# Performance work log

Measured on AMD Instinct MI355X. Metric: run time of the kernel, lower is better.

The kernel has to match this reference:

```python
import jax, jax.numpy as jnp
import numpy as np

N_NODES = 8192
K = 32

def setup_inputs() -> dict:
    key = jax.random.key(0)
    kA, kI = jax.random.split(key)
    A = jax.random.normal(kA, (N_NODES, N_NODES), dtype=jnp.float32)
    idx = jnp.arange(N_NODES, dtype=jnp.int64)  # unused by forward, kept for signature fidelity
    return {"A": A, "idx": idx}

def reference(A, idx):
    # adj = relu(A)
    adj = jax.nn.relu(A)
    # row-wise top-k indices, scatter 1.0 into a zero mask, multiply
    _, indices = jax.lax.top_k(adj, K)            # [N, K]
    rows = jnp.arange(adj.shape[0])[:, None]      # [N, 1]
    mask = jnp.zeros_like(adj).at[rows, indices].set(1.0)
    return adj * mask
```

## Files before the change

kernel.cpp:

```cpp
#include <hip/hip_runtime.h>


constexpr int N     = 8192;
constexpr int K     = 32;
constexpr int NBINS = 2048;
constexpr int SPEC_BASE = 1024;
constexpr int CAP   = 512;
constexpr int SLOTS = CAP / 64;
constexpr int BB    = 128;
constexpr int BLOCK = 256;
constexpr float TSPEC = 2.0f;

typedef float f4 __attribute__((ext_vector_type(4)));

template<int PER>
__device__ __forceinline__ bool find_cutoff(const unsigned* hist, int lane,
                                            int base, int& B, int& G) {
    unsigned s = 0;
    #pragma unroll
    for (int i = 0; i < PER; ++i)
        s += hist[base + lane * PER + ((i + lane) & (PER - 1))];
    unsigned acc = s;
    #pragma unroll
    for (int off = 1; off < 64; off <<= 1) {
        unsigned t = __shfl_down(acc, off, 64);
        if (lane + off < 64) acc += t;
    }
    unsigned long long m = __ballot(acc >= (unsigned)K);
    if (m == 0ull) return false;
    int g = 63 - __clzll((long long)m);
    unsigned above = (g < 63) ? (unsigned)__shfl((int)acc, g + 1, 64) : 0u;
    unsigned h  = (lane < PER) ? hist[base + g * PER + lane] : 0u;
    unsigned a2 = h;
    #pragma unroll
    for (int off = 1; off < 64; off <<= 1) {
        unsigned t = __shfl_down(a2, off, 64);
        if (lane + off < 64) a2 += t;
    }
    unsigned long long m2 = __ballot(above + a2 >= (unsigned)K);
    int bl = 63 - __clzll((long long)m2);
    B = base + g * PER + bl;
    G = (int)(above + (unsigned)__shfl((int)a2, bl, 64)
                    - (unsigned)__shfl((int)h,  bl, 64));
    return true;
}

__global__ __launch_bounds__(BLOCK)
void topk_relu_kernel(const float* __restrict__ A, float* __restrict__ Out) {
    const int row  = blockIdx.x;
    const int tid  = threadIdx.x;
    const int lane = tid & 63;
    const int wave = tid >> 6;

    __shared__ unsigned hist[NBINS];
    __shared__ float    cv[CAP];
    __shared__ int      cc[CAP];
    __shared__ float    bbv[BB];
    __shared__ int      bbc[BB];
    __shared__ unsigned ccnt;

    #pragma unroll
    for (int i = 0; i < (NBINS - SPEC_BASE) / BLOCK; ++i)
        hist[SPEC_BASE + tid + i * BLOCK] = 0u;
    if (tid == 0) ccnt = 0u;
    __syncthreads();

    const f4* __restrict__ Arow = reinterpret_cast<const f4*>(A + (size_t)row * N);
    #pragma unroll
    for (int i = 0; i < 8; ++i) {
        f4 v = Arow[i * BLOCK + tid];
        #pragma unroll
        for (int c = 0; c < 4; ++c) {
            float f = v[c];
            if (f > TSPEC) {
                atomicAdd(&hist[__float_as_uint(f) >> 20], 1u);
                unsigned ix = atomicAdd(&ccnt, 1u);
                if (ix < CAP) { cv[ix] = f; cc[ix] = (i * BLOCK + tid) * 4 + c; }
            }
        }
    }
    __syncthreads();

    int B, G;
    bool ok = find_cutoff<16>(hist, lane, SPEC_BASE, B, G);
    const unsigned Call = ccnt;
    f4* __restrict__ Orow4 = reinterpret_cast<f4*>(Out + (size_t)row * N);

    if (ok && Call <= (unsigned)CAP) {
        const f4 z = {0.0f, 0.0f, 0.0f, 0.0f};
        #pragma unroll
        for (int i = 0; i < 8; ++i)
            __builtin_nontemporal_store(z, Orow4 + i * BLOCK + tid);

        const int R = K - G;
        const int C = (int)Call;
        int total = 0;
        #pragma unroll
        for (int s = 0; s < SLOTS; ++s) {
            const int j = lane + s * 64;
            bool flag = false; float fv = 0.0f; int fc = 0;
            if (j < C) {
                fv = cv[j];
                if ((int)(__float_as_uint(fv) >> 20) == B) { flag = true; fc = cc[j]; }
            }
            unsigned long long m = __ballot(flag);
            if (flag) {
                int pos = total + __popcll(m & ((1ull << lane) - 1ull));
                if (pos < BB) { bbv[pos] = fv; bbc[pos] = fc; }
            }
            total += (int)__popcll(m);
        }
        const int T = min(total, BB);
        float mv0 = -1.0f, mv1 = -1.0f; int mc0 = 0x7fffffff, mc1 = 0x7fffffff;
        if (lane      < T) { mv0 = bbv[lane];      mc0 = bbc[lane]; }
        if (lane + 64 < T) { mv1 = bbv[lane + 64]; mc1 = bbc[lane + 64]; }
        int r0 = 0, r1 = 0;
        for (int j = 0; j < T; ++j) {
            const float vj = bbv[j];
            const int   cj = bbc[j];
            if (vj > mv0 || (vj == mv0 && cj < mc0)) r0++;
            if (vj > mv1 || (vj == mv1 && cj < mc1)) r1++;
        }
        float bv = 0.0f; int bc = -1; bool found = false;
        if (lane      < T && r0 == R - 1) { bv = mv0; bc = mc0; found = true; }
        if (lane + 64 < T && r1 == R - 1) { bv = mv1; bc = mc1; found = true; }
        float vR = __int_as_float(0x7f800000);
        int   cR = -1;
        unsigned long long bm = __ballot(found);
        if (bm != 0ull) {
            int src = (int)__ffsll((long long)bm) - 1;
            vR = __shfl(bv, src, 64);
            cR = __shfl(bc, src, 64);
        }

        __syncthreads();

        if (wave == 0) {
            float* __restrict__ Orow = Out + (size_t)row * N;
            #pragma unroll
            for (int s = 0; s < SLOTS; ++s) {
                const int j = lane + s * 64;
                if (j < C) {
                    float f = cv[j]; int c = cc[j];
                    if (f > vR || (f == vR && c <= cR)) Orow[c] = f;
                }
            }
        }
        return;
    }

    __syncthreads();
    #pragma unroll
    for (int i = 0; i < NBINS / BLOCK; ++i) hist[tid + i * BLOCK] = 0u;
    if (tid == 0) ccnt = 0u;
    __syncthreads();
    #pragma unroll
    for (int i = 0; i < 8; ++i) {
        f4 v = Arow[i * BLOCK + tid];
        #pragma unroll
        for (int c = 0; c < 4; ++c) {
            float f = v[c];
            if (f > 0.0f) atomicAdd(&hist[__float_as_uint(f) >> 20], 1u);
        }
    }
    __syncthreads();
    if (!find_cutoff<32>(hist, lane, 0, B, G)) { B = -1; G = 0; }
    if (B >= 0) {
        #pragma unroll
        for (int i = 0; i < 8; ++i) {
            f4 v = Arow[i * BLOCK + tid];
            #pragma unroll
            for (int c = 0; c < 4; ++c) {
                float f = v[c];
                if (f > 0.0f && (int)(__float_as_uint(f) >> 20) == B) {
                    unsigned ix = atomicAdd(&ccnt, 1u);
                    if (ix < CAP) { cv[ix] = f; cc[ix] = (i * BLOCK + tid) * 4 + c; }
                }
            }
        }
    }
    __syncthreads();

    float vR = 0.0f;
    int   cR = -1;
    if (B >= 0) {
        const int R = K - G;
        const int C = (int)min(ccnt, (unsigned)CAP);
        float mv[SLOTS]; int mc[SLOTS]; int rk[SLOTS];
        #pragma unroll
        for (int s = 0; s < SLOTS; ++s) {
            const int j = lane + s * 64;
            if (j < C) { mv[s] = cv[j]; mc[s] = cc[j]; }
            else       { mv[s] = -1.0f; mc[s] = 0x7fffffff; }
            rk[s] = 0;
        }
        for (int j = 0; j < C; ++j) {
            const float vj = cv[j];
            const int   cj = cc[j];
            #pragma unroll
            for (int s = 0; s < SLOTS; ++s)
                if (vj > mv[s] || (vj == mv[s] && cj < mc[s])) rk[s]++;
        }
        float bv = 0.0f; int bc = -1; bool found = false;
        #pragma unroll
        for (int s = 0; s < SLOTS; ++s)
            if (lane + s * 64 < C && rk[s] == R - 1) { bv = mv[s]; bc = mc[s]; found = true; }
        vR = __int_as_float(0x7f800000);
        unsigned long long bm = __ballot(found);
        if (bm != 0ull) {
            int src = (int)__ffsll((long long)bm) - 1;
            vR = __shfl(bv, src, 64);
            cR = __shfl(bc, src, 64);
        }
    }

    #pragma unroll
    for (int i = 0; i < 8; ++i) {
        f4 v = Arow[i * BLOCK + tid];
        f4 w;
        #pragma unroll
        for (int c = 0; c < 4; ++c) {
            float f   = v[c];
            int   col = (i * BLOCK + tid) * 4 + c;
            w[c] = ((f > vR) || (f == vR && col <= cR)) ? f : 0.0f;
        }
        __builtin_nontemporal_store(w, Orow4 + i * BLOCK + tid);
    }
}

extern "C" void kernel_launch(void* const* d_in, const int* in_sizes, int n_in,
                              void* d_out, int out_size, void* d_ws, size_t ws_size,
                              hipStream_t stream) {
    const float* A   = (const float*)d_in[0];
    float*       Out = (float*)d_out;
    (void)in_sizes; (void)n_in; (void)d_ws; (void)ws_size; (void)out_size;
    topk_relu_kernel<<<dim3(N), dim3(BLOCK), 0, stream>>>(A, Out);
}
```

Before: 104.7 us.

## Write fast-path output as full vector stores with winners merged per thread

In the speculative fast path, only wave 0 now computes the cutoff. It then routes each selected top-k element into a per-thread shared slot keyed by the output vector that thread owns. After one barrier, every thread writes its row segment as full float4 nontemporal stores with the winners merged in. This replaces writing zeros and then scattering scalar stores to the same lines, and it removes a barrier and the redundant cutoff work in the other waves. The cost is extra shared memory and a fallback to the slow path when a thread receives more than four winners or the bucket overflows.

```diff
diff --git a/kernel.cpp b/kernel.cpp
--- a/kernel.cpp
+++ b/kernel.cpp
@@ -9,6 +9,7 @@
 constexpr int SLOTS = CAP / 64;
 constexpr int BB    = 128;
 constexpr int BLOCK = 256;
+constexpr int PSLOT = 4;
 constexpr float TSPEC = 2.0f;
 
 typedef float f4 __attribute__((ext_vector_type(4)));
@@ -57,12 +58,17 @@
     __shared__ int      cc[CAP];
     __shared__ float    bbv[BB];
     __shared__ int      bbc[BB];
+    __shared__ float    pval[PSLOT][BLOCK];
+    __shared__ int      pcol[PSLOT][BLOCK];
+    __shared__ unsigned pcnt[BLOCK];
     __shared__ unsigned ccnt;
+    __shared__ int      fb;
 
     #pragma unroll
     for (int i = 0; i < (NBINS - SPEC_BASE) / BLOCK; ++i)
         hist[SPEC_BASE + tid + i * BLOCK] = 0u;
-    if (tid == 0) ccnt = 0u;
+    pcnt[tid] = 0u;
+    if (tid == 0) { ccnt = 0u; fb = 0; }
     __syncthreads();
 
     const f4* __restrict__ Arow = reinterpret_cast<const f4*>(A + (size_t)row * N);
@@ -81,75 +87,111 @@
     }
     __syncthreads();
 
-    int B, G;
-    bool ok = find_cutoff<16>(hist, lane, SPEC_BASE, B, G);
-    const unsigned Call = ccnt;
     f4* __restrict__ Orow4 = reinterpret_cast<f4*>(Out + (size_t)row * N);
 
-    if (ok && Call <= (unsigned)CAP) {
-        const f4 z = {0.0f, 0.0f, 0.0f, 0.0f};
-        #pragma unroll
-        for (int i = 0; i < 8; ++i)
-            __builtin_nontemporal_store(z, Orow4 + i * BLOCK + tid);
-
-        const int R = K - G;
-        const int C = (int)Call;
-        int total = 0;
-        #pragma unroll
-        for (int s = 0; s < SLOTS; ++s) {
-            const int j = lane + s * 64;
-            bool flag = false; float fv = 0.0f; int fc = 0;
-            if (j < C) {
-                fv = cv[j];
-                if ((int)(__float_as_uint(fv) >> 20) == B) { flag = true; fc = cc[j]; }
-            }
-            unsigned long long m = __ballot(flag);
-            if (flag) {
-                int pos = total + __popcll(m & ((1ull << lane) - 1ull));
-                if (pos < BB) { bbv[pos] = fv; bbc[pos] = fc; }
-            }
-            total += (int)__popcll(m);
-        }
-        const int T = min(total, BB);
-        float mv0 = -1.0f, mv1 = -1.0f; int mc0 = 0x7fffffff, mc1 = 0x7fffffff;
-        if (lane      < T) { mv0 = bbv[lane];      mc0 = bbc[lane]; }
-        if (lane + 64 < T) { mv1 = bbv[lane + 64]; mc1 = bbc[lane + 64]; }
-        int r0 = 0, r1 = 0;
-        for (int j = 0; j < T; ++j) {
-            const float vj = bbv[j];
-            const int   cj = bbc[j];
-            if (vj > mv0 || (vj == mv0 && cj < mc0)) r0++;
-            if (vj > mv1 || (vj == mv1 && cj < mc1)) r1++;
-        }
-        float bv = 0.0f; int bc = -1; bool found = false;
-        if (lane      < T && r0 == R - 1) { bv = mv0; bc = mc0; found = true; }
-        if (lane + 64 < T && r1 == R - 1) { bv = mv1; bc = mc1; found = true; }
-        float vR = __int_as_float(0x7f800000);
-        int   cR = -1;
-        unsigned long long bm = __ballot(found);
-        if (bm != 0ull) {
-            int src = (int)__ffsll((long long)bm) - 1;
-            vR = __shfl(bv, src, 64);
-            cR = __shfl(bc, src, 64);
-        }
-
-        __syncthreads();
-
-        if (wave == 0) {
-            float* __restrict__ Orow = Out + (size_t)row * N;
+    if (wave == 0) {
+        int B, G;
+        bool ok = find_cutoff<16>(hist, lane, SPEC_BASE, B, G);
+        const unsigned Call = ccnt;
+        if (!ok || Call > (unsigned)CAP) {
+            fb = 1;
+        } else {
+            const int R = K - G;
+            const int C = (int)Call;
+            int total = 0;
             #pragma unroll
             for (int s = 0; s < SLOTS; ++s) {
                 const int j = lane + s * 64;
+                bool flag = false; float fv = 0.0f; int fc = 0;
                 if (j < C) {
-                    float f = cv[j]; int c = cc[j];
-                    if (f > vR || (f == vR && c <= cR)) Orow[c] = f;
-                }
-            }
+                    fv = cv[j];
+                    if ((int)(__float_as_uint(fv) >> 20) == B) { flag = true; fc = cc[j]; }
+                }
+                unsigned long long m = __ballot(flag);
+                if (flag) {
+                    int pos = total + __popcll(m & ((1ull << lane) - 1ull));
+                    if (pos < BB) { bbv[pos] = fv; bbc[pos] = fc; }
+                }
+                total += (int)__popcll(m);
+            }
+            if (total > BB) {
+                fb = 1;
+            } else {
+                const int T = total;
+                float mv0 = -1.0f, mv1 = -1.0f; int mc0 = 0x7fffffff, mc1 = 0x7fffffff;
+                if (lane      < T) { mv0 = bbv[lane];      mc0 = bbc[lane]; }
+                if (lane + 64 < T) { mv1 = bbv[lane + 64]; mc1 = bbc[lane + 64]; }
+                int r0 = 0, r1 = 0;
+                for (int j = 0; j < T; ++j) {
+                    const float vj = bbv[j];
+                    const int   cj = bbc[j];
+                    if (vj > mv0 || (vj == mv0 && cj < mc0)) r0++;
+                    if (vj > mv1 || (vj == mv1 && cj < mc1)) r1++;
+                }
+                float bv = 0.0f; int bc = -1; bool found = false;
+                if (lane      < T && r0 == R - 1) { bv = mv0; bc = mc0; found = true; }
+                if (lane + 64 < T && r1 == R - 1) { bv = mv1; bc = mc1; found = true; }
+                float vR = __int_as_float(0x7f800000);
+                int   cR = -1;
+                unsigned long long bm = __ballot(found);
+                if (bm != 0ull) {
+                    int src = (int)__ffsll((long long)bm) - 1;
+                    vR = __shfl(bv, src, 64);
+                    cR = __shfl(bc, src, 64);
+                }
+                #pragma unroll
+                for (int s = 0; s < SLOTS; ++s) {
+                    const int j = lane + s * 64;
+                    if (j < C) {
+                        float fv = cv[j]; int fc = cc[j];
+                        if (fv > vR || (fv == vR && fc <= cR)) {
+                            int owner = (fc >> 2) & (BLOCK - 1);
+                            unsigned p = atomicAdd(&pcnt[owner], 1u);
+                            if (p < (unsigned)PSLOT) {
+                                pval[p][owner] = fv;
+                                pcol[p][owner] = fc;
+                            } else {
+                                fb = 1;
+                            }
+                        }
+                    }
+                }
+            }
+        }
+    }
+    __syncthreads();
+
+    if (!fb) {
+        const unsigned cnt = pcnt[tid];
+        const float v0 = pval[0][tid], v1 = pval[1][tid],
+                    v2 = pval[2][tid], v3 = pval[3][tid];
+        const int   c0 = pcol[0][tid], c1 = pcol[1][tid],
+                    c2 = pcol[2][tid], c3 = pcol[3][tid];
+        unsigned m8 = 0;
+        if (cnt > 0) m8 |= 1u << (c0 >> 10);
+        if (cnt > 1) m8 |= 1u << (c1 >> 10);
+        if (cnt > 2) m8 |= 1u << (c2 >> 10);
+        if (cnt > 3) m8 |= 1u << (c3 >> 10);
+        #pragma unroll
+        for (int i = 0; i < 8; ++i) {
+            f4 w = {0.0f, 0.0f, 0.0f, 0.0f};
+            if (m8 & (1u << i)) {
+                #define APPLY(CC, VV, KI)                                          \
+                    if (cnt > (KI) && ((CC) >> 10) == i) {                         \
+                        const int cm = (CC) & 3;                                   \
+                        w[0] = (cm == 0) ? (VV) : w[0];                            \
+                        w[1] = (cm == 1) ? (VV) : w[1];                            \
+                        w[2] = (cm == 2) ? (VV) : w[2];                            \
+                        w[3] = (cm == 3) ? (VV) : w[3];                            \
+                    }
+                APPLY(c0, v0, 0) APPLY(c1, v1, 1) APPLY(c2, v2, 2) APPLY(c3, v3, 3)
+                #undef APPLY
+            }
+            __builtin_nontemporal_store(w, Orow4 + i * BLOCK + tid);
         }
         return;
     }
 
-    __syncthreads();
     #pragma unroll
     for (int i = 0; i < NBINS / BLOCK; ++i) hist[tid + i * BLOCK] = 0u;
     if (tid == 0) ccnt = 0u;
@@ -164,6 +206,7 @@
         }
     }
     __syncthreads();
+    int B, G;
     if (!find_cutoff<32>(hist, lane, 0, B, G)) { B = -1; G = 0; }
     if (B >= 0) {
         #pragma unroll
```

After: 91.94 us. 1.14x faster.
